# Optimization experiments

Hardware: AMD Instinct MI355X
Metric: run time of the kernel (lower is better)

Reference implementation:

```python
import jax, jax.numpy as jnp
import numpy as np
from jax import lax

B, C, H, W = 32, 1, 512, 512

def kernel_gauss_2d(m=3, sigma=3):
    x = np.arange(-m, m + 0.1)
    X, Y = np.meshgrid(x, x)
    g = np.exp(-(X ** 2 + Y ** 2) / (2 * sigma ** 2))
    g /= np.sum(g)
    return g.astype(np.float32)

KERNEL33 = (0.25 * np.array([[0., 1., 0.], [1., 0., 1.], [0., 1., 0.]], dtype=np.float32))
KERNEL_GAUSS = kernel_gauss_2d(m=3, sigma=3)  # 7x7


def _conv(x, w, pad):
    # NCHW conv, stride 1, symmetric padding
    return lax.conv_general_dilated(
        x, w, window_strides=(1, 1), padding=[(pad, pad), (pad, pad)],
        dimension_numbers=("NCHW", "OIHW", "NCHW"))


def _maxpool(x, k, pad):
    return lax.reduce_window(
        x, -jnp.inf, lax.max,
        window_dimensions=(1, 1, k, k), window_strides=(1, 1, 1, 1),
        padding=[(0, 0), (0, 0), (pad, pad), (pad, pad)])


def setup_inputs() -> dict:
    key = jax.random.key(0)
    ks = jax.random.split(key, 9)
    d = {"X": jax.random.normal(ks[0], (B, C, H, W), dtype=jnp.float32)}
    d["w0"] = jax.random.normal(ks[1], (2, 1, 1, 1), dtype=jnp.float32) * 0.5
    d["b0"] = jax.random.normal(ks[2], (2,), dtype=jnp.float32) * 0.1
    for i in range(1, 7):
        d[f"w{i}"] = jax.random.normal(ks[2 + i], (2, 1, 1, 1), dtype=jnp.float32) * 0.5
    return d


def reference(X, w0, b0, w1, w2, w3, w4, w5, w6):
    k33 = jnp.asarray(KERNEL33).reshape(1, 1, 3, 3)
    kg = jnp.asarray(KERNEL_GAUSS).reshape(1, 1, 7, 7)

    X1 = _conv(X, k33, pad=1)                 # fixed 3x3 blur
    X2 = _conv(X, kg, pad=3)                  # fixed 7x7 gaussian
    X3 = -_maxpool(-X, 3, pad=1)              # 3x3 min-pool
    X4 = -_maxpool(-X, 11, pad=5)             # 11x11 min-pool
    X5 = _maxpool(X, 3, pad=1)                # 3x3 max-pool
    X6 = _maxpool(X, 11, pad=5)               # 11x11 max-pool

    out = _conv(X, w0, 0) + b0.reshape(1, 2, 1, 1)
    out = out + _conv(X1, w1, 0) + _conv(X2, w2, 0) + _conv(X3, w3, 0)
    out = out + _conv(X4, w4, 0) + _conv(X5, w5, 0) + _conv(X6, w6, 0)
    return out
```

## Files before the change

### kernel.cpp

```cpp
#include <hip/hip_runtime.h>

#define IMG 512
#define TW 64
#define TH 32
#define PROWS 42
#define GST 64
#define RST 72

typedef __fp16 h2v __attribute__((ext_vector_type(2)));
union UH { unsigned u; h2v h; };
union US { unsigned short s; __fp16 h; };

__device__ __forceinline__ float nan0(float v){ return v==v ? v : 0.0f; }
__device__ __forceinline__ float min3f(float a,float b,float c){ return fminf(fminf(a,b),c); }
__device__ __forceinline__ float max3f(float a,float b,float c){ return fmaxf(fmaxf(a,b),c); }

__global__ __launch_bounds__(512, 8)
void simplenet_fused(const float* __restrict__ X,
                     const float* __restrict__ w0, const float* __restrict__ b0,
                     const float* __restrict__ w1, const float* __restrict__ w2,
                     const float* __restrict__ w3, const float* __restrict__ w4,
                     const float* __restrict__ w5, const float* __restrict__ w6,
                     float* __restrict__ out)
{
    __shared__ unsigned       HNX[PROWS*GST];
    __shared__ unsigned short GHH[38*GST];
    __shared__ float          RAW[35*RST];

    const int tid = threadIdx.x;
    const int xo = tid & 63, ty = tid >> 6, y0 = ty*4;
    const int bx = blockIdx.x, by = blockIdx.y, bz = blockIdx.z;
    const int tx0 = bx*TW, ty0 = by*TH;
    const bool xe = (bx==0)||(bx==IMG/TW-1);
    const bool ye = (by==0)||(by==IMG/TH-1);
    const float* Xb = X + (size_t)bz*(IMG*IMG);
    const float qn = __builtin_nanf("");

    const float W0c0=w0[0], W0c1=w0[1], B0=b0[0], B1=b0[1];
    const float W1c0=w1[0], W1c1=w1[1], W2c0=w2[0], W2c1=w2[1];
    const float W3c0=w3[0], W3c1=w3[1], W4c0=w4[0], W4c1=w4[1];
    const float W5c0=w5[0], W5c1=w5[1], W6c0=w6[0], W6c1=w6[1];

    const float G0=0.10628875f, G1=0.14032194f, G2=0.16577342f, G3=0.17523179f;

    auto load_task = [&](int t, float* x) -> bool {
        const int r = t >> 4, g = t & 15;
        const int gy  = ty0 - 5 + r;
        const int gx0 = tx0 - 8 + 4*g;
        if ((unsigned)gy >= IMG) return true;
        const bool xs = (unsigned)gx0 > (unsigned)(IMG-20);
        if (!xs) {
#pragma unroll
            for (int j=0;j<5;++j) {
                const float4 q = *(const float4*)(Xb + gy*IMG + gx0 + 4*j);
                x[4*j]=q.x; x[4*j+1]=q.y; x[4*j+2]=q.z; x[4*j+3]=q.w;
            }
        } else {
            const float* row = Xb + gy*IMG;
#pragma unroll
            for (int i=0;i<20;++i) {
                const int gx = gx0 + i;
                const float v = row[min(max(gx,0),IMG-1)];
                x[i] = ((unsigned)gx < IMG) ? v : qn;
            }
        }
        return false;
    };
    auto compute_task = [&](int t, const float* x, bool oob) {
        const int r = t >> 4, g = t & 15;
        const int wb = r*GST + 4*g;
        const bool rawrow = (r >= 4 && r <= 38);
        if (oob) {
            *(uint4*)&HNX[wb] = make_uint4(0x7BFF7BFFu,0x7BFF7BFFu,0x7BFF7BFFu,0x7BFF7BFFu);
            if (r >= 2 && r < 40)
                *(uint2*)&GHH[(r-2)*GST+4*g] = make_uint2(0u,0u);
            if (rawrow) {
                *(float4*)&RAW[(r-4)*RST + 4*g + 4] = make_float4(qn,qn,qn,qn);
                if (g==0)  RAW[(r-4)*RST + 3]  = qn;
                if (g==15) RAW[(r-4)*RST + 68] = qn;
            }
            return;
        }
        if (rawrow) {
            *(float4*)&RAW[(r-4)*RST + 4*g + 4] = make_float4(x[8],x[9],x[10],x[11]);
            if (g==0)  RAW[(r-4)*RST + 3]  = x[7];
            if (g==15) RAW[(r-4)*RST + 68] = x[12];
        }
        float mn[12], mx[12];
#pragma unroll
        for (int i=0;i<12;++i) {
            mn[i] = min3f(x[i+3],x[i+4],x[i+5]);
            mx[i] = max3f(x[i+3],x[i+4],x[i+5]);
        }
        unsigned hw[4];
#pragma unroll
        for (int k=0;k<4;++k) {
            const float hn = fminf(fminf(mn[k],mn[k+3]), fminf(mn[k+6],mn[k+8]));
            const float hx = fmaxf(fmaxf(mx[k],mx[k+3]), fmaxf(mx[k+6],mx[k+8]));
            UH c; c.h = __builtin_amdgcn_cvt_pkrtz(hn, -hx);
            hw[k] = c.u;
        }
        *(uint4*)&HNX[wb] = make_uint4(hw[0],hw[1],hw[2],hw[3]);
        if (r >= 2 && r < 40) {
            const bool xs = (unsigned)(tx0 - 8 + 4*g) > (unsigned)(IMG-20);
            float zz[10];
#pragma unroll
            for (int j=0;j<10;++j) zz[j] = xs ? nan0(x[5+j]) : x[5+j];
            float gh[4];
#pragma unroll
            for (int k=0;k<4;++k)
                gh[k] = G0*(zz[k]+zz[k+6]) + G1*(zz[k+1]+zz[k+5]) + G2*(zz[k+2]+zz[k+4]) + G3*zz[k+3];
            UH c01, c23;
            c01.h = __builtin_amdgcn_cvt_pkrtz(gh[0], gh[1]);
            c23.h = __builtin_amdgcn_cvt_pkrtz(gh[2], gh[3]);
            *(uint2*)&GHH[(r-2)*GST+4*g] = make_uint2(c01.u, c23.u);
        }
    };

    float x0[20], x1[20];
    const bool has1 = tid < (PROWS*16 - 512);
    const bool oob0 = load_task(tid, x0);
    bool oob1 = true;
    if (has1) oob1 = load_task(512 + tid, x1);
    compute_task(tid, x0, oob0);
    if (has1) compute_task(512 + tid, x1, oob1);

    __syncthreads();

    float a0[4], a1[4];

    {
        float L[6], C[6], R[6];
#pragma unroll
        for (int i=0;i<6;++i) {
            const int base = (y0+i)*RST + xo + 4;
            L[i]=RAW[base-1]; C[i]=RAW[base]; R[i]=RAW[base+1];
        }
        h2v q[14];
#pragma unroll
        for (int i=0;i<14;++i) { UH u; u.u = HNX[(y0+i)*GST+xo]; q[i] = u.h; }
        float wv[10];
#pragma unroll
        for (int i=0;i<10;++i) { US u; u.s = GHH[(y0+i)*GST+xo]; wv[i] = (float)u.h; }

        float hm[6], hx6[6];
#pragma unroll
        for (int i=0;i<6;++i) { hm[i]=min3f(L[i],C[i],R[i]); hx6[i]=max3f(L[i],C[i],R[i]); }
        float Lz[6], Rz[6];
#pragma unroll
        for (int i=0;i<6;++i) { Lz[i] = xe ? nan0(L[i]) : L[i];
                                Rz[i] = xe ? nan0(R[i]) : R[i]; }
        const float Cz0 = ye ? nan0(C[0]) : C[0];
        const float Cz5 = ye ? nan0(C[5]) : C[5];
        const float up[4]={Cz0,C[1],C[2],C[3]};
        const float dn[4]={C[2],C[3],C[4],Cz5};
#pragma unroll
        for (int p=0;p<4;++p) {
            const float cr = 0.25f*(up[p] + dn[p] + Lz[p+1] + Rz[p+1]);
            a0[p] = B0 + W0c0*C[p+1] + W1c0*cr;
            a1[p] = B1 + W0c1*C[p+1] + W1c1*cr;
            const float mnv = min3f(hm[p],hm[p+1],hm[p+2]);
            const float mxv = max3f(hx6[p],hx6[p+1],hx6[p+2]);
            a0[p] += W3c0*mnv + W5c0*mxv;
            a1[p] += W3c1*mnv + W5c1*mxv;
        }

#pragma unroll
        for (int p=0;p<4;++p) {
            const float s = G0*(wv[p]+wv[p+6]) + G1*(wv[p+1]+wv[p+5])
                          + G2*(wv[p+2]+wv[p+4]) + G3*wv[p+3];
            a0[p] += W2c0*s; a1[p] += W2c1*s;
        }

        h2v s = q[10];
#pragma unroll
        for (int i=9;i>=4;--i) s = __builtin_elementwise_min(s, q[i]);
        const h2v S3 = __builtin_elementwise_min(s,  q[3]);
        const h2v S2 = __builtin_elementwise_min(S3, q[2]);
        const h2v S1 = __builtin_elementwise_min(S2, q[1]);
        const h2v S0 = __builtin_elementwise_min(S1, q[0]);
        const h2v p1 = q[11];
        const h2v p2 = __builtin_elementwise_min(p1, q[12]);
        const h2v p3 = __builtin_elementwise_min(p2, q[13]);
        const h2v o0 = S0;
        const h2v o1 = __builtin_elementwise_min(S1, p1);
        const h2v o2 = __builtin_elementwise_min(S2, p2);
        const h2v o3 = __builtin_elementwise_min(S3, p3);
        const float on[4] = {(float)o0[0], (float)o1[0], (float)o2[0], (float)o3[0]};
        const float ox[4] = {-(float)o0[1], -(float)o1[1], -(float)o2[1], -(float)o3[1]};
#pragma unroll
        for (int p=0;p<4;++p) {
            a0[p] += W4c0*on[p] + W6c0*ox[p];
            a1[p] += W4c1*on[p] + W6c1*ox[p];
        }
    }

    float* o0p = out + ((size_t)bz*2 + 0)*(IMG*IMG) + (size_t)(ty0+y0)*IMG + tx0 + xo;
    float* o1p = o0p + (IMG*IMG);
#pragma unroll
    for (int p=0;p<4;++p) {
        o0p[(size_t)p*IMG] = a0[p];
        o1p[(size_t)p*IMG] = a1[p];
    }
}

extern "C" void kernel_launch(void* const* d_in, const int* in_sizes, int n_in,
                              void* d_out, int out_size, void* d_ws, size_t ws_size,
                              hipStream_t stream) {
    const float* X  = (const float*)d_in[0];
    const float* w0 = (const float*)d_in[1];
    const float* b0 = (const float*)d_in[2];
    const float* w1 = (const float*)d_in[3];
    const float* w2 = (const float*)d_in[4];
    const float* w3 = (const float*)d_in[5];
    const float* w4 = (const float*)d_in[6];
    const float* w5 = (const float*)d_in[7];
    const float* w6 = (const float*)d_in[8];
    float* out = (float*)d_out;

    dim3 grid(IMG/TW, IMG/TH, 32);
    simplenet_fused<<<grid, 512, 0, stream>>>(X, w0, b0, w1, w2, w3, w4, w5, w6, out);
}
```

Before: 37.46 us.

## Make blocks loop over four tiles, prefetching next tile during compute

```diff
diff --git a/kernel.cpp b/kernel.cpp
--- a/kernel.cpp
+++ b/kernel.cpp
@@ -6,6 +6,7 @@
 #define PROWS 42
 #define GST 64
 #define RST 72
+#define NTILE 4
 
 typedef __fp16 h2v __attribute__((ext_vector_type(2)));
 union UH { unsigned u; h2v h; };
@@ -29,21 +30,15 @@
 
     const int tid = threadIdx.x;
     const int xo = tid & 63, ty = tid >> 6, y0 = ty*4;
-    const int bx = blockIdx.x, by = blockIdx.y, bz = blockIdx.z;
-    const int tx0 = bx*TW, ty0 = by*TH;
-    const bool xe = (bx==0)||(bx==IMG/TW-1);
-    const bool ye = (by==0)||(by==IMG/TH-1);
-    const float* Xb = X + (size_t)bz*(IMG*IMG);
     const float qn = __builtin_nanf("");
 
     const float W0c0=w0[0], W0c1=w0[1], B0=b0[0], B1=b0[1];
     const float W1c0=w1[0], W1c1=w1[1], W2c0=w2[0], W2c1=w2[1];
     const float W3c0=w3[0], W3c1=w3[1], W4c0=w4[0], W4c1=w4[1];
     const float W5c0=w5[0], W5c1=w5[1], W6c0=w6[0], W6c1=w6[1];
-
     const float G0=0.10628875f, G1=0.14032194f, G2=0.16577342f, G3=0.17523179f;
 
-    auto load_task = [&](int t, float* x) -> bool {
+    auto load_task = [&](int t, const float* Xb, int tx0, int ty0, float* x) -> bool {
         const int r = t >> 4, g = t & 15;
         const int gy  = ty0 - 5 + r;
         const int gx0 = tx0 - 8 + 4*g;
@@ -66,7 +61,7 @@
         }
         return false;
     };
-    auto compute_task = [&](int t, const float* x, bool oob) {
+    auto compute_task = [&](int t, const float* x, bool oob, int tx0) {
         const int r = t >> 4, g = t & 15;
         const int wb = r*GST + 4*g;
         const bool rawrow = (r >= 4 && r <= 38);
@@ -117,90 +112,112 @@
         }
     };
 
-    float x0[20], x1[20];
     const bool has1 = tid < (PROWS*16 - 512);
-    const bool oob0 = load_task(tid, x0);
-    bool oob1 = true;
-    if (has1) oob1 = load_task(512 + tid, x1);
-    compute_task(tid, x0, oob0);
-    if (has1) compute_task(512 + tid, x1, oob1);
-
-    __syncthreads();
-
-    float a0[4], a1[4];
-
-    {
-        float L[6], C[6], R[6];
-#pragma unroll
-        for (int i=0;i<6;++i) {
-            const int base = (y0+i)*RST + xo + 4;
-            L[i]=RAW[base-1]; C[i]=RAW[base]; R[i]=RAW[base+1];
-        }
-        h2v q[14];
-#pragma unroll
-        for (int i=0;i<14;++i) { UH u; u.u = HNX[(y0+i)*GST+xo]; q[i] = u.h; }
-        float wv[10];
-#pragma unroll
-        for (int i=0;i<10;++i) { US u; u.s = GHH[(y0+i)*GST+xo]; wv[i] = (float)u.h; }
-
-        float hm[6], hx6[6];
-#pragma unroll
-        for (int i=0;i<6;++i) { hm[i]=min3f(L[i],C[i],R[i]); hx6[i]=max3f(L[i],C[i],R[i]); }
-        float Lz[6], Rz[6];
-#pragma unroll
-        for (int i=0;i<6;++i) { Lz[i] = xe ? nan0(L[i]) : L[i];
-                                Rz[i] = xe ? nan0(R[i]) : R[i]; }
-        const float Cz0 = ye ? nan0(C[0]) : C[0];
-        const float Cz5 = ye ? nan0(C[5]) : C[5];
-        const float up[4]={Cz0,C[1],C[2],C[3]};
-        const float dn[4]={C[2],C[3],C[4],Cz5};
+
+    int tx0, ty0, bz; bool xe, ye; const float* Xb;
+    auto decode = [&](int t) {
+        const int bx = t & 7, by = (t >> 3) & 15;
+        bz = t >> 7;
+        tx0 = bx*TW; ty0 = by*TH;
+        xe = (bx==0)||(bx==7); ye = (by==0)||(by==15);
+        Xb = X + (size_t)bz*(IMG*IMG);
+    };
+
+    const int t0 = blockIdx.x * NTILE;
+    decode(t0);
+    float x0[20];
+    bool oob0 = load_task(tid, Xb, tx0, ty0, x0);
+
+    for (int i = 0; i < NTILE; ++i) {
+        float x1[20]; bool oob1 = true;
+        if (has1) oob1 = load_task(512 + tid, Xb, tx0, ty0, x1);
+        compute_task(tid, x0, oob0, tx0);
+        if (has1) compute_task(512 + tid, x1, oob1, tx0);
+
+        const int stx0 = tx0, sty0 = ty0, sbz = bz;
+        const bool sxe = xe, sye = ye;
+
+        __syncthreads();
+
+        if (i + 1 < NTILE) {
+            decode(t0 + i + 1);
+            oob0 = load_task(tid, Xb, tx0, ty0, x0);
+        }
+
+        float a0[4], a1[4];
+        {
+            float L[6], C[6], R[6];
+#pragma unroll
+            for (int k=0;k<6;++k) {
+                const int base = (y0+k)*RST + xo + 4;
+                L[k]=RAW[base-1]; C[k]=RAW[base]; R[k]=RAW[base+1];
+            }
+            h2v q[14];
+#pragma unroll
+            for (int k=0;k<14;++k) { UH u; u.u = HNX[(y0+k)*GST+xo]; q[k] = u.h; }
+            float wv[10];
+#pragma unroll
+            for (int k=0;k<10;++k) { US u; u.s = GHH[(y0+k)*GST+xo]; wv[k] = (float)u.h; }
+
+            float hm[6], hx6[6];
+#pragma unroll
+            for (int k=0;k<6;++k) { hm[k]=min3f(L[k],C[k],R[k]); hx6[k]=max3f(L[k],C[k],R[k]); }
+            float Lz[6], Rz[6];
+#pragma unroll
+            for (int k=0;k<6;++k) { Lz[k] = sxe ? nan0(L[k]) : L[k];
+                                    Rz[k] = sxe ? nan0(R[k]) : R[k]; }
+            const float Cz0 = sye ? nan0(C[0]) : C[0];
+            const float Cz5 = sye ? nan0(C[5]) : C[5];
+            const float up[4]={Cz0,C[1],C[2],C[3]};
+            const float dn[4]={C[2],C[3],C[4],Cz5};
+#pragma unroll
+            for (int p=0;p<4;++p) {
+                const float cr = 0.25f*(up[p] + dn[p] + Lz[p+1] + Rz[p+1]);
+                a0[p] = B0 + W0c0*C[p+1] + W1c0*cr;
+                a1[p] = B1 + W0c1*C[p+1] + W1c1*cr;
+                const float mnv = min3f(hm[p],hm[p+1],hm[p+2]);
+                const float mxv = max3f(hx6[p],hx6[p+1],hx6[p+2]);
+                a0[p] += W3c0*mnv + W5c0*mxv;
+                a1[p] += W3c1*mnv + W5c1*mxv;
+            }
+#pragma unroll
+            for (int p=0;p<4;++p) {
+                const float s = G0*(wv[p]+wv[p+6]) + G1*(wv[p+1]+wv[p+5])
+                              + G2*(wv[p+2]+wv[p+4]) + G3*wv[p+3];
+                a0[p] += W2c0*s; a1[p] += W2c1*s;
+            }
+            h2v s = q[10];
+#pragma unroll
+            for (int k=9;k>=4;--k) s = __builtin_elementwise_min(s, q[k]);
+            const h2v S3 = __builtin_elementwise_min(s,  q[3]);
+            const h2v S2 = __builtin_elementwise_min(S3, q[2]);
+            const h2v S1 = __builtin_elementwise_min(S2, q[1]);
+            const h2v S0 = __builtin_elementwise_min(S1, q[0]);
+            const h2v p1 = q[11];
+            const h2v p2 = __builtin_elementwise_min(p1, q[12]);
+            const h2v p3 = __builtin_elementwise_min(p2, q[13]);
+            const h2v o0 = S0;
+            const h2v o1 = __builtin_elementwise_min(S1, p1);
+            const h2v o2 = __builtin_elementwise_min(S2, p2);
+            const h2v o3 = __builtin_elementwise_min(S3, p3);
+            const float on[4] = {(float)o0[0], (float)o1[0], (float)o2[0], (float)o3[0]};
+            const float ox[4] = {-(float)o0[1], -(float)o1[1], -(float)o2[1], -(float)o3[1]};
+#pragma unroll
+            for (int p=0;p<4;++p) {
+                a0[p] += W4c0*on[p] + W6c0*ox[p];
+                a1[p] += W4c1*on[p] + W6c1*ox[p];
+            }
+        }
+
+        float* o0p = out + ((size_t)sbz*2 + 0)*(IMG*IMG) + (size_t)(sty0+y0)*IMG + stx0 + xo;
+        float* o1p = o0p + (IMG*IMG);
 #pragma unroll
         for (int p=0;p<4;++p) {
-            const float cr = 0.25f*(up[p] + dn[p] + Lz[p+1] + Rz[p+1]);
-            a0[p] = B0 + W0c0*C[p+1] + W1c0*cr;
-            a1[p] = B1 + W0c1*C[p+1] + W1c1*cr;
-            const float mnv = min3f(hm[p],hm[p+1],hm[p+2]);
-            const float mxv = max3f(hx6[p],hx6[p+1],hx6[p+2]);
-            a0[p] += W3c0*mnv + W5c0*mxv;
-            a1[p] += W3c1*mnv + W5c1*mxv;
-        }
-
-#pragma unroll
-        for (int p=0;p<4;++p) {
-            const float s = G0*(wv[p]+wv[p+6]) + G1*(wv[p+1]+wv[p+5])
-                          + G2*(wv[p+2]+wv[p+4]) + G3*wv[p+3];
-            a0[p] += W2c0*s; a1[p] += W2c1*s;
-        }
-
-        h2v s = q[10];
-#pragma unroll
-        for (int i=9;i>=4;--i) s = __builtin_elementwise_min(s, q[i]);
-        const h2v S3 = __builtin_elementwise_min(s,  q[3]);
-        const h2v S2 = __builtin_elementwise_min(S3, q[2]);
-        const h2v S1 = __builtin_elementwise_min(S2, q[1]);
-        const h2v S0 = __builtin_elementwise_min(S1, q[0]);
-        const h2v p1 = q[11];
-        const h2v p2 = __builtin_elementwise_min(p1, q[12]);
-        const h2v p3 = __builtin_elementwise_min(p2, q[13]);
-        const h2v o0 = S0;
-        const h2v o1 = __builtin_elementwise_min(S1, p1);
-        const h2v o2 = __builtin_elementwise_min(S2, p2);
-        const h2v o3 = __builtin_elementwise_min(S3, p3);
-        const float on[4] = {(float)o0[0], (float)o1[0], (float)o2[0], (float)o3[0]};
-        const float ox[4] = {-(float)o0[1], -(float)o1[1], -(float)o2[1], -(float)o3[1]};
-#pragma unroll
-        for (int p=0;p<4;++p) {
-            a0[p] += W4c0*on[p] + W6c0*ox[p];
-            a1[p] += W4c1*on[p] + W6c1*ox[p];
-        }
-    }
-
-    float* o0p = out + ((size_t)bz*2 + 0)*(IMG*IMG) + (size_t)(ty0+y0)*IMG + tx0 + xo;
-    float* o1p = o0p + (IMG*IMG);
-#pragma unroll
-    for (int p=0;p<4;++p) {
-        o0p[(size_t)p*IMG] = a0[p];
-        o1p[(size_t)p*IMG] = a1[p];
+            o0p[(size_t)p*IMG] = a0[p];
+            o1p[(size_t)p*IMG] = a1[p];
+        }
+
+        __syncthreads();
     }
 }
 
@@ -218,6 +235,6 @@
     const float* w6 = (const float*)d_in[8];
     float* out = (float*)d_out;
 
-    dim3 grid(IMG/TW, IMG/TH, 32);
-    simplenet_fused<<<grid, 512, 0, stream>>>(X, w0, b0, w1, w2, w3, w4, w5, w6, out);
+    const int ntiles = (IMG/TW) * (IMG/TH) * 32;
+    simplenet_fused<<<ntiles / NTILE, 512, 0, stream>>>(X, w0, b0, w1, w2, w3, w4, w5, w6, out);
 }
```

Measured after the change: 89.54 us. 2.39x slower.
